# Kernel optimization log

Hardware: AMD Instinct MI355X
Metric: run time of the kernel (lower is better)

The kernel has to match this reference:

```python
import jax, jax.numpy as jnp
import numpy as np

N_NODES = 100000
N_EDGES = 1600000
F_IN = 256
HID = 16
HEADS = 8
N_CLASSES = 16
NEG_SLOPE = 0.2  # DGL GATConv default leaky_relu slope


def setup_inputs() -> dict:
    key = jax.random.key(0)
    ks = jax.random.split(key, 12)
    feat = jax.random.normal(ks[0], (N_NODES, F_IN), dtype=jnp.float32)
    src = jax.random.randint(ks[1], (N_EDGES,), 0, N_NODES, dtype=jnp.int32)
    dst = jax.random.randint(ks[2], (N_EDGES,), 0, N_NODES, dtype=jnp.int32)
    s1 = 1.0 / np.sqrt(F_IN)
    s2 = 1.0 / np.sqrt(HID * HEADS)
    W1 = jax.random.normal(ks[3], (F_IN, HEADS * HID), dtype=jnp.float32) * s1
    al1 = jax.random.normal(ks[4], (HEADS, HID), dtype=jnp.float32) * s1
    ar1 = jax.random.normal(ks[5], (HEADS, HID), dtype=jnp.float32) * s1
    b1 = jnp.zeros((HEADS * HID,), dtype=jnp.float32)
    W2 = jax.random.normal(ks[6], (HEADS * HID, N_CLASSES), dtype=jnp.float32) * s2
    al2 = jax.random.normal(ks[7], (1, N_CLASSES), dtype=jnp.float32) * s2
    ar2 = jax.random.normal(ks[8], (1, N_CLASSES), dtype=jnp.float32) * s2
    b2 = jnp.zeros((N_CLASSES,), dtype=jnp.float32)
    return {"feat": feat, "src": src, "dst": dst,
            "W1": W1, "al1": al1, "ar1": ar1, "b1": b1,
            "W2": W2, "al2": al2, "ar2": ar2, "b2": b2}


def gat_conv(x, src, dst, W, attn_l, attn_r, bias, n_heads, out_dim):
    # x: [N, F_in]; W: [F_in, H*D]; attn_l/attn_r: [H, D]; bias: [H*D]
    n = x.shape[0]
    h = (x @ W).reshape(n, n_heads, out_dim)              # [N,H,D]
    el = jnp.einsum('nhd,hd->nh', h, attn_l)              # [N,H]
    er = jnp.einsum('nhd,hd->nh', h, attn_r)              # [N,H]
    e = jax.nn.leaky_relu(el[src] + er[dst], NEG_SLOPE)   # [E,H]
    # segment softmax over incoming edges of each destination node
    e_max = jax.ops.segment_max(e, dst, num_segments=n)   # [N,H] (-inf for isolated)
    ex = jnp.exp(e - e_max[dst])                          # [E,H]
    denom = jax.ops.segment_sum(ex, dst, num_segments=n)  # [N,H]
    a = ex / denom[dst]                                   # [E,H]
    msg = a[:, :, None] * h[src]                          # [E,H,D]
    out = jax.ops.segment_sum(msg, dst, num_segments=n)   # [N,H,D]
    return out + bias.reshape(1, n_heads, out_dim)


def reference(feat, src, dst, W1, al1, ar1, b1, W2, al2, ar2, b2):
    h = gat_conv(feat, src, dst, W1, al1, ar1, b1, HEADS, HID)   # [N,H,HID]
    h = jax.nn.elu(h.reshape(h.shape[0], -1))                     # [N,H*HID]
    h = gat_conv(h, src, dst, W2, al2, ar2, b2, 1, N_CLASSES)     # [N,1,C]
    h = h.reshape(h.shape[0], -1)
    return jax.nn.log_softmax(h, axis=1)
```

## Files before the change

### kernel.cpp

```cpp
#include <hip/hip_runtime.h>

#define N_NODES 100000
#define N_EDGES 1600000
#define F_IN 256
#define HD1 128
#define HEADS 8
#define HID 16
#define NC 16
#define NEG_SLOPE 0.2f
#define LOG2E 1.44269504f

#define BKT_NODES 512
#define NBKT ((N_NODES + BKT_NODES - 1) / BKT_NODES)
#define P1_EPB 8192
#define P1_BLOCKS ((N_EDGES + P1_EPB - 1) / P1_EPB)

__device__ __forceinline__ float leaky(float x){ return x > 0.f ? x : NEG_SLOPE * x; }
__device__ __forceinline__ unsigned short f2bf(float f){
    unsigned u = __float_as_uint(f);
    u += 0x7fff + ((u >> 16) & 1);
    return (unsigned short)(u >> 16);
}
__device__ __forceinline__ float bf2f(unsigned short s){
    return __uint_as_float((unsigned)s << 16);
}
__device__ __forceinline__ unsigned char f2fp8(float v){
    return (unsigned char)(__builtin_amdgcn_cvt_pk_fp8_f32(v, v, 0, false) & 0xff);
}
__device__ __forceinline__ unsigned cvtpk_bf16(float lo, float hi){
    unsigned r;
    asm("v_cvt_pk_bf16_f32 %0, %1, %2" : "=v"(r) : "v"(lo), "v"(hi));
    return r;
}

typedef __bf16 bf16x8 __attribute__((ext_vector_type(8)));
typedef short short8 __attribute__((ext_vector_type(8)));
typedef float f32x4 __attribute__((ext_vector_type(4)));
typedef float f32x2 __attribute__((ext_vector_type(2)));


__global__ void __launch_bounds__(256) k_p1hist(const int* __restrict__ dst, int* __restrict__ bucketTotal){
    __shared__ int h[NBKT];
    int t = threadIdx.x;
    for (int i = t; i < NBKT; i += 256) h[i] = 0;
    __syncthreads();
    int base = blockIdx.x * P1_EPB;
    int m = min(P1_EPB, N_EDGES - base);
    for (int i = t; i < m; i += 256) atomicAdd(&h[(unsigned)dst[base + i] >> 9], 1);
    __syncthreads();
    for (int i = t; i < NBKT; i += 256) if (h[i]) atomicAdd(&bucketTotal[i], h[i]);
}

__global__ void __launch_bounds__(256) k_p1scan(const int* __restrict__ bucketTotal,
                                                int* __restrict__ bucketBase, int* __restrict__ bucketCursor,
                                                int* __restrict__ off){
    __shared__ int sc[256];
    int t = threadIdx.x;
    int v = (t < NBKT) ? bucketTotal[t] : 0;
    sc[t] = v; __syncthreads();
    for (int o = 1; o < 256; o <<= 1){
        int a = (t >= o) ? sc[t - o] : 0;
        __syncthreads();
        sc[t] += a;
        __syncthreads();
    }
    if (t < NBKT){
        int b = sc[t] - v;
        bucketBase[t] = b;
        bucketCursor[t] = b;
    }
    if (t == 0){ bucketBase[NBKT] = N_EDGES; off[N_NODES] = N_EDGES; }
}

__global__ void __launch_bounds__(256) k_p1bin(const int* __restrict__ src, const int* __restrict__ dst,
                                               int* __restrict__ bucketCursor,
                                               unsigned long long* __restrict__ pairs){
    __shared__ unsigned long long pl[P1_EPB];
    __shared__ int h[NBKT];
    __shared__ int dl[NBKT];
    __shared__ int sc[256];
    int t = threadIdx.x;
    for (int i = t; i < NBKT; i += 256) h[i] = 0;
    __syncthreads();
    int base = blockIdx.x * P1_EPB;
    int m = min(P1_EPB, N_EDGES - base);
    for (int i = t; i < m; i += 256) atomicAdd(&h[(unsigned)dst[base + i] >> 9], 1);
    __syncthreads();
    int v = (t < NBKT) ? h[t] : 0;
    sc[t] = v; __syncthreads();
    for (int o = 1; o < 256; o <<= 1){
        int a = (t >= o) ? sc[t - o] : 0;
        __syncthreads();
        sc[t] += a;
        __syncthreads();
    }
    if (t < NBKT){
        int ex = sc[t] - v;
        int gb = v ? atomicAdd(&bucketCursor[t], v) : 0;
        dl[t] = gb - ex;
        h[t] = ex;
    }
    __syncthreads();
    for (int i = t; i < m; i += 256){
        int d = dst[base + i], s = src[base + i];
        int b = (unsigned)d >> 9;
        int p = atomicAdd(&h[b], 1);
        pl[p] = ((unsigned long long)(unsigned)d << 32) | (unsigned)s;
    }
    __syncthreads();
    for (int i = t; i < m; i += 256){
        unsigned long long pr = pl[i];
        int b = (unsigned)(pr >> 32) >> 9;
        pairs[i + dl[b]] = pr;
    }
}

__global__ void __launch_bounds__(256) k_p2place(const unsigned long long* __restrict__ pairs,
                                                 const int* __restrict__ bucketBase,
                                                 int* __restrict__ off, int* __restrict__ csr_src){
    __shared__ int degc[BKT_NODES];
    __shared__ int sc2[BKT_NODES];
    int t = threadIdx.x;
    int b = blockIdx.x;
    int node0 = b * BKT_NODES;
    int nmax = min(BKT_NODES, N_NODES - node0);
    int p0 = bucketBase[b], p1 = bucketBase[b + 1];
    int m = p1 - p0;
    for (int i = t; i < BKT_NODES; i += 256) degc[i] = 0;
    __syncthreads();
    for (int i = t; i < m; i += 256){
        int d = (int)(pairs[p0 + i] >> 32) - node0;
        atomicAdd(&degc[d], 1);
    }
    __syncthreads();
    for (int i = t; i < BKT_NODES; i += 256) sc2[i] = degc[i];
    __syncthreads();
    for (int o = 1; o < BKT_NODES; o <<= 1){
        int i0 = t, i1 = t + 256;
        int a0 = (i0 >= o) ? sc2[i0 - o] : 0;
        int a1 = (i1 >= o) ? sc2[i1 - o] : 0;
        __syncthreads();
        sc2[i0] += a0; sc2[i1] += a1;
        __syncthreads();
    }
    for (int i = t; i < BKT_NODES; i += 256){
        int cur = p0 + sc2[i] - degc[i];
        if (i < nmax) off[node0 + i] = cur;
        degc[i] = cur;
    }
    __syncthreads();
    for (int i = t; i < m; i += 256){
        unsigned long long pr = pairs[p0 + i];
        int d = (int)(pr >> 32) - node0;
        int pos = atomicAdd(&degc[d], 1);
        csr_src[pos] = (int)(unsigned)pr;
    }
}


__global__ void __launch_bounds__(256) k_splitW(const float* __restrict__ W1,
                                                short* __restrict__ WTH){
    int i = blockIdx.x * 256 + threadIdx.x;
    if (i >= F_IN * HD1) return;
    int k = i >> 7, n = i & 127;
    int idx = n * 256 + (k ^ ((n & 7) << 3));
    WTH[idx] = (short)f2bf(W1[i]);
}


__device__ __forceinline__ short8 pack8(float4 f0, float4 f1){
    uint4 p;
    p.x = cvtpk_bf16(f0.x, f0.y);
    p.y = cvtpk_bf16(f0.z, f0.w);
    p.z = cvtpk_bf16(f1.x, f1.y);
    p.w = cvtpk_bf16(f1.z, f1.w);
    return __builtin_bit_cast(short8, p);
}

__global__ void __launch_bounds__(256, 2) k_gemm1m(const float* __restrict__ feat,
                                                   const short* __restrict__ WTH,
                                                   unsigned char* __restrict__ h1f8){
    __shared__ short sWH[64 * 256];
    int t = threadIdx.x;
    int ch = blockIdx.y;
    {
        const short8* gh = (const short8*)(WTH + (size_t)ch * 16384);
        short8* sh = (short8*)sWH;
        for (int i = t; i < 2048; i += 256) sh[i] = gh[i];
    }

    int wid = t >> 6, lane = t & 63;
    int m16 = lane & 15, kg = lane >> 4;
    int rowb = blockIdx.x * 128 + wid * 32;

    int r0 = rowb + m16;       if (r0 > N_NODES - 1) r0 = N_NODES - 1;
    int r1 = rowb + 16 + m16;  if (r1 > N_NODES - 1) r1 = N_NODES - 1;
    const float* fp0 = feat + (size_t)r0 * F_IN;
    const float* fp1 = feat + (size_t)r1 * F_IN;

    float4 s0[16], s1[16];
    #pragma unroll
    for (int ks = 0; ks < 8; ks++){
        const float4* p = (const float4*)(fp0 + ks * 32 + kg * 8);
        s0[2 * ks] = p[0]; s0[2 * ks + 1] = p[1];
    }
    #pragma unroll
    for (int ks = 0; ks < 8; ks++){
        const float4* p = (const float4*)(fp1 + ks * 32 + kg * 8);
        s1[2 * ks] = p[0]; s1[2 * ks + 1] = p[1];
    }

    __syncthreads();

    f32x4 acc[2][4];
    #pragma unroll
    for (int a = 0; a < 2; a++)
        #pragma unroll
        for (int b = 0; b < 4; b++)
            acc[a][b] = (f32x4){0.f, 0.f, 0.f, 0.f};

    #pragma unroll
    for (int ks = 0; ks < 8; ks++){
        int kbase = ks * 32 + kg * 8;
        bf16x8 AH0 = __builtin_bit_cast(bf16x8, pack8(s0[2 * ks], s0[2 * ks + 1]));
        bf16x8 AH1 = __builtin_bit_cast(bf16x8, pack8(s1[2 * ks], s1[2 * ks + 1]));
        #pragma unroll
        for (int c = 0; c < 4; c++){
            int n = (c << 4) + m16;
            int kk = kbase ^ ((n & 7) << 3);
            bf16x8 bh = __builtin_bit_cast(bf16x8, *(const short8*)(sWH + n * 256 + kk));
            acc[0][c] = __builtin_amdgcn_mfma_f32_16x16x32_bf16(AH0, bh, acc[0][c], 0, 0, 0);
            acc[1][c] = __builtin_amdgcn_mfma_f32_16x16x32_bf16(AH1, bh, acc[1][c], 0, 0, 0);
        }
    }

    #pragma unroll
    for (int rf = 0; rf < 2; rf++){
        #pragma unroll
        for (int c = 0; c < 4; c++){
            #pragma unroll
            for (int r = 0; r < 4; r++){
                int row = rowb + rf * 16 + kg * 4 + r;
                if (row < N_NODES){
                    int col = ch * 64 + c * 16 + m16;
                    h1f8[(size_t)row * HD1 + col] = f2fp8(acc[rf][c][r]);
                }
            }
        }
    }
}


__global__ void __launch_bounds__(256) k_attn1(const unsigned char* __restrict__ h1f8,
                                               const float* __restrict__ al1, const float* __restrict__ ar1,
                                               unsigned short* __restrict__ el1b, float* __restrict__ er1){
    int i = blockIdx.x * 256 + threadIdx.x;
    if (i >= N_NODES * HEADS) return;
    int n = i >> 3, h = i & 7;
    const unsigned* hp = (const unsigned*)(h1f8 + (size_t)n * HD1 + h * HID);
    float pe = 0.f, pr = 0.f;
    #pragma unroll
    for (int j = 0; j < 4; j++){
        unsigned u = hp[j];
        float x0 = __builtin_amdgcn_cvt_f32_fp8(u, 0);
        float x1 = __builtin_amdgcn_cvt_f32_fp8(u, 1);
        float x2 = __builtin_amdgcn_cvt_f32_fp8(u, 2);
        float x3 = __builtin_amdgcn_cvt_f32_fp8(u, 3);
        const float4 a = ((const float4*)(al1 + h * HID))[j];
        const float4 r = ((const float4*)(ar1 + h * HID))[j];
        pe += x0 * a.x + x1 * a.y + x2 * a.z + x3 * a.w;
        pr += x0 * r.x + x1 * r.y + x2 * r.z + x3 * r.w;
    }
    el1b[i] = f2bf(pe * LOG2E);
    er1[i] = pr * LOG2E;
}


__global__ void __launch_bounds__(256) k_agg1(const int* __restrict__ off, const int* __restrict__ csr_src,
                                              const unsigned short* __restrict__ el1b,
                                              const float* __restrict__ er1,
                                              const unsigned char* __restrict__ h1f8,
                                              const float* __restrict__ b1,
                                              unsigned short* __restrict__ x2b){
    int wid = threadIdx.x >> 6, lane = threadIdx.x & 63;
    int n = blockIdx.x * 4 + wid;
    if (n >= N_NODES) return;
    int jb = off[n], je = off[n + 1];
    int sub = lane >> 4;
    int q = lane & 15;
    int hh = q >> 1;
    float ern = er1[n * HEADS + hh];
    float a0=0.f,a1=0.f,a2=0.f,a3=0.f,a4=0.f,a5=0.f,a6=0.f,a7=0.f,wsum=0.f;

    #pragma unroll 2
    for (int j = jb; j < je; j += 4){
        int jj = j + sub;
        int jc = (jj < je) ? jj : je - 1;
        int s = csr_src[jc];
        float el = bf2f(el1b[s * HEADS + hh]);
        float wv = (jj < je) ? __builtin_amdgcn_exp2f(leaky(el + ern)) : 0.f;
        wsum += wv;
        uint2 u = *(const uint2*)(h1f8 + (((size_t)s) << 7) + (q << 3));
        f32x2 p0 = __builtin_amdgcn_cvt_pk_f32_fp8(u.x, 0);
        f32x2 p1 = __builtin_amdgcn_cvt_pk_f32_fp8(u.x, 1);
        f32x2 p2 = __builtin_amdgcn_cvt_pk_f32_fp8(u.y, 0);
        f32x2 p3 = __builtin_amdgcn_cvt_pk_f32_fp8(u.y, 1);
        a0 += wv * p0.x; a1 += wv * p0.y;
        a2 += wv * p1.x; a3 += wv * p1.y;
        a4 += wv * p2.x; a5 += wv * p2.y;
        a6 += wv * p3.x; a7 += wv * p3.y;
    }

    a0 += __shfl_xor(a0, 16); a0 += __shfl_xor(a0, 32);
    a1 += __shfl_xor(a1, 16); a1 += __shfl_xor(a1, 32);
    a2 += __shfl_xor(a2, 16); a2 += __shfl_xor(a2, 32);
    a3 += __shfl_xor(a3, 16); a3 += __shfl_xor(a3, 32);
    a4 += __shfl_xor(a4, 16); a4 += __shfl_xor(a4, 32);
    a5 += __shfl_xor(a5, 16); a5 += __shfl_xor(a5, 32);
    a6 += __shfl_xor(a6, 16); a6 += __shfl_xor(a6, 32);
    a7 += __shfl_xor(a7, 16); a7 += __shfl_xor(a7, 32);
    wsum += __shfl_xor(wsum, 16); wsum += __shfl_xor(wsum, 32);

    if (sub == 0){
        float inv = (je > jb) ? 1.f / wsum : 0.f;
        float o0 = a0*inv, o1 = a1*inv, o2 = a2*inv, o3 = a3*inv;
        float o4 = a4*inv, o5 = a5*inv, o6 = a6*inv, o7 = a7*inv;
        float4 bv0 = *(const float4*)(b1 + (q << 3));
        float4 bv1 = *(const float4*)(b1 + (q << 3) + 4);
        o0 += bv0.x; o1 += bv0.y; o2 += bv0.z; o3 += bv0.w;
        o4 += bv1.x; o5 += bv1.y; o6 += bv1.z; o7 += bv1.w;
        o0 = o0 > 0.f ? o0 : __expf(o0) - 1.f;
        o1 = o1 > 0.f ? o1 : __expf(o1) - 1.f;
        o2 = o2 > 0.f ? o2 : __expf(o2) - 1.f;
        o3 = o3 > 0.f ? o3 : __expf(o3) - 1.f;
        o4 = o4 > 0.f ? o4 : __expf(o4) - 1.f;
        o5 = o5 > 0.f ? o5 : __expf(o5) - 1.f;
        o6 = o6 > 0.f ? o6 : __expf(o6) - 1.f;
        o7 = o7 > 0.f ? o7 : __expf(o7) - 1.f;
        uint4 ov;
        ov.x = cvtpk_bf16(o0, o1);
        ov.y = cvtpk_bf16(o2, o3);
        ov.z = cvtpk_bf16(o4, o5);
        ov.w = cvtpk_bf16(o6, o7);
        *(uint4*)(x2b + (size_t)n * HD1 + (q << 3)) = ov;
    }
}


__global__ void __launch_bounds__(256) k_gemm2(const unsigned short* __restrict__ x2b, const float* __restrict__ W2,
                                               const float* __restrict__ al2, const float* __restrict__ ar2,
                                               unsigned short* __restrict__ h2b, float* __restrict__ el2, float* __restrict__ er2){
    __shared__ float sW[HD1 * NC];
    __shared__ float sX[16 * HD1];
    int t = threadIdx.x;
    for (int i = t; i < (HD1 * NC) / 4; i += 256)
        ((float4*)sW)[i] = ((const float4*)W2)[i];
    int r = t >> 4, c = t & 15;
    float a2 = al2[c], r2 = ar2[c];
    for (int g = blockIdx.x; g * 16 < N_NODES; g += gridDim.x){
        int rowb = g * 16;
        __syncthreads();
        {
            ushort4 v = ((const ushort4*)(x2b + (size_t)rowb * HD1))[t * 2];
            ushort4 v2 = ((const ushort4*)(x2b + (size_t)rowb * HD1))[t * 2 + 1];
            float4 f0 = { bf2f(v.x), bf2f(v.y), bf2f(v.z), bf2f(v.w) };
            float4 f1 = { bf2f(v2.x), bf2f(v2.y), bf2f(v2.z), bf2f(v2.w) };
            ((float4*)sX)[t * 2] = f0;
            ((float4*)sX)[t * 2 + 1] = f1;
        }
        __syncthreads();
        float acc = 0.f;
        #pragma unroll 8
        for (int k = 0; k < HD1; k++)
            acc += sX[r * HD1 + k] * sW[k * NC + c];
        int row = rowb + r;
        h2b[row * NC + c] = f2bf(acc);
        float pe = acc * a2, pr = acc * r2;
        #pragma unroll
        for (int d = 1; d < 16; d <<= 1){ pe += __shfl_xor(pe, d); pr += __shfl_xor(pr, d); }
        if (c == 0){ el2[row] = pe * LOG2E; er2[row] = pr * LOG2E; }
    }
}


__global__ void __launch_bounds__(256) k_agg2(const int* __restrict__ off, const int* __restrict__ csr_src,
                                              const float* __restrict__ el2, const float* __restrict__ er2,
                                              const unsigned short* __restrict__ h2b, const float* __restrict__ b2,
                                              float* __restrict__ out){
    int t = threadIdx.x;
    int sub = t >> 4;
    int c = t & 15;
    int n = blockIdx.x * 16 + sub;
    if (n >= N_NODES) return;
    int jb = off[n], je = off[n + 1];
    float er = er2[n];
    float accA = 0.f, accB = 0.f, wsA = 0.f, wsB = 0.f;
    int j = jb;
    for (; j + 1 < je; j += 2){
        int s0 = csr_src[j];
        int s1 = csr_src[j + 1];
        float w0 = __builtin_amdgcn_exp2f(leaky(el2[s0] + er));
        float w1 = __builtin_amdgcn_exp2f(leaky(el2[s1] + er));
        float v0 = bf2f(h2b[(size_t)s0 * NC + c]);
        float v1 = bf2f(h2b[(size_t)s1 * NC + c]);
        wsA += w0; accA += w0 * v0;
        wsB += w1; accB += w1 * v1;
    }
    if (j < je){
        int s0 = csr_src[j];
        float w0 = __builtin_amdgcn_exp2f(leaky(el2[s0] + er));
        wsA += w0; accA += w0 * bf2f(h2b[(size_t)s0 * NC + c]);
    }
    float acc = accA + accB, wsum = wsA + wsB;
    float o = (je > jb) ? acc / wsum : 0.f;
    o += b2[c];
    float m = o;
    #pragma unroll
    for (int d = 1; d < 16; d <<= 1) m = fmaxf(m, __shfl_xor(m, d));
    float ex = __expf(o - m);
    #pragma unroll
    for (int d = 1; d < 16; d <<= 1) ex += __shfl_xor(ex, d);
    out[(size_t)n * NC + c] = o - m - __logf(ex);
}


extern "C" void kernel_launch(void* const* d_in, const int* in_sizes, int n_in,
                              void* d_out, int out_size, void* d_ws, size_t ws_size,
                              hipStream_t stream){
    const float* feat = (const float*)d_in[0];
    const int*   src  = (const int*)d_in[1];
    const int*   dst  = (const int*)d_in[2];
    const float* W1   = (const float*)d_in[3];
    const float* al1  = (const float*)d_in[4];
    const float* ar1  = (const float*)d_in[5];
    const float* b1   = (const float*)d_in[6];
    const float* W2   = (const float*)d_in[7];
    const float* al2  = (const float*)d_in[8];
    const float* ar2  = (const float*)d_in[9];
    const float* b2   = (const float*)d_in[10];
    float* out = (float*)d_out;

    char* w = (char*)d_ws;
    auto alloc = [&](size_t bytes) -> char* {
        char* p = w;
        w += (bytes + 255) & ~(size_t)255;
        return p;
    };
    int*   off      = (int*)alloc((size_t)(N_NODES + 1) * 4);
    int*   csr_src  = (int*)alloc((size_t)N_EDGES * 4);
    unsigned long long* pairs = (unsigned long long*)alloc((size_t)N_EDGES * 8);
    int*   bucketTotal  = (int*)alloc((size_t)(NBKT + 1) * 4);
    int*   bucketBase   = (int*)alloc((size_t)(NBKT + 1) * 4);
    int*   bucketCursor = (int*)alloc((size_t)(NBKT + 1) * 4);
    unsigned char*  h1f8 = (unsigned char*)alloc((size_t)N_NODES * HD1);
    unsigned short* el1b = (unsigned short*)alloc((size_t)N_NODES * HEADS * 2);
    float* er1v    = (float*)alloc((size_t)N_NODES * HEADS * 4);
    unsigned short* x2b = (unsigned short*)alloc((size_t)N_NODES * HD1 * 2);
    unsigned short* h2b = (unsigned short*)alloc((size_t)N_NODES * NC * 2);
    float* el2v    = (float*)alloc((size_t)N_NODES * 4);
    float* er2v    = (float*)alloc((size_t)N_NODES * 4);
    short* WTH     = (short*)alloc((size_t)F_IN * HD1 * 2);

    hipMemsetAsync(bucketTotal, 0, (size_t)(NBKT + 1) * 4, stream);
    k_p1hist<<<P1_BLOCKS, 256, 0, stream>>>(dst, bucketTotal);
    k_p1scan<<<1, 256, 0, stream>>>(bucketTotal, bucketBase, bucketCursor, off);
    k_p1bin<<<P1_BLOCKS, 256, 0, stream>>>(src, dst, bucketCursor, pairs);
    k_p2place<<<NBKT, 256, 0, stream>>>(pairs, bucketBase, off, csr_src);

    k_splitW<<<(F_IN * HD1 + 255) / 256, 256, 0, stream>>>(W1, WTH);
    dim3 g1((N_NODES + 127) / 128, 2);
    k_gemm1m<<<g1, 256, 0, stream>>>(feat, WTH, h1f8);
    k_attn1<<<(N_NODES * HEADS + 255) / 256, 256, 0, stream>>>(h1f8, al1, ar1, el1b, er1v);

    k_agg1<<<(N_NODES + 3) / 4, 256, 0, stream>>>(off, csr_src, el1b, er1v, h1f8, b1, x2b);

    k_gemm2<<<1024, 256, 0, stream>>>(x2b, W2, al2, ar2, h2b, el2v, er2v);
    k_agg2<<<(N_NODES + 15) / 16, 256, 0, stream>>>(off, csr_src, el2v, er2v, h2b, b2, out);
}
```

Measured before the change: 234.1 us.

## Compute all 128 GEMM1 columns per block with LDS-staged, double-buffered features

The first-layer GEMM now has each block compute all 128 output columns instead of splitting them across two column-chunk blocks, so each feature row is read from global memory once rather than twice. Feature tiles are streamed into a swizzled, double-buffered LDS array using direct global-to-LDS loads, which replaces the large per-thread register prefetch. The costs are a larger LDS footprint (the full bf16 weight plus two feature buffers, about 96KB), which limits occupancy, a __syncthreads per k-step, and twice as many accumulators per wave.

```diff
diff --git a/kernel.cpp b/kernel.cpp
--- a/kernel.cpp
+++ b/kernel.cpp
@@ -32,6 +32,11 @@
     asm("v_cvt_pk_bf16_f32 %0, %1, %2" : "=v"(r) : "v"(lo), "v"(hi));
     return r;
 }
+__device__ __forceinline__ void gload_lds16(const float* g, float* l){
+    __builtin_amdgcn_global_load_lds(
+        (const __attribute__((address_space(1))) unsigned int*)g,
+        (__attribute__((address_space(3))) unsigned int*)l, 16, 0, 0);
+}
 
 typedef __bf16 bf16x8 __attribute__((ext_vector_type(8)));
 typedef short short8 __attribute__((ext_vector_type(8)));
@@ -177,72 +182,82 @@
     return __builtin_bit_cast(short8, p);
 }
 
-__global__ void __launch_bounds__(256, 2) k_gemm1m(const float* __restrict__ feat,
-                                                   const short* __restrict__ WTH,
-                                                   unsigned char* __restrict__ h1f8){
-    __shared__ short sWH[64 * 256];
-    int t = threadIdx.x;
-    int ch = blockIdx.y;
+__global__ void __launch_bounds__(256) k_gemm1m(const float* __restrict__ feat,
+                                                const short* __restrict__ WTH,
+                                                unsigned char* __restrict__ h1f8){
+    __shared__ short sWH[F_IN * HD1];
+    __shared__ float sF[2][4096];
+    int t = threadIdx.x;
     {
-        const short8* gh = (const short8*)(WTH + (size_t)ch * 16384);
+        const short8* gh = (const short8*)WTH;
         short8* sh = (short8*)sWH;
-        for (int i = t; i < 2048; i += 256) sh[i] = gh[i];
+        for (int i = t; i < 4096; i += 256) sh[i] = gh[i];
     }
 
     int wid = t >> 6, lane = t & 63;
     int m16 = lane & 15, kg = lane >> 4;
-    int rowb = blockIdx.x * 128 + wid * 32;
-
-    int r0 = rowb + m16;       if (r0 > N_NODES - 1) r0 = N_NODES - 1;
-    int r1 = rowb + 16 + m16;  if (r1 > N_NODES - 1) r1 = N_NODES - 1;
-    const float* fp0 = feat + (size_t)r0 * F_IN;
-    const float* fp1 = feat + (size_t)r1 * F_IN;
-
-    float4 s0[16], s1[16];
-    #pragma unroll
-    for (int ks = 0; ks < 8; ks++){
-        const float4* p = (const float4*)(fp0 + ks * 32 + kg * 8);
-        s0[2 * ks] = p[0]; s0[2 * ks + 1] = p[1];
-    }
-    #pragma unroll
-    for (int ks = 0; ks < 8; ks++){
-        const float4* p = (const float4*)(fp1 + ks * 32 + kg * 8);
-        s1[2 * ks] = p[0]; s1[2 * ks + 1] = p[1];
-    }
-
-    __syncthreads();
-
-    f32x4 acc[2][4];
+    int rowb = blockIdx.x * 128;
+
+    int srow = lane >> 3;
+    int scg  = (lane & 7) ^ srow;
+
+    auto stage = [&](int ks, int b){
+        #pragma unroll
+        for (int i = 0; i < 4; i++){
+            int reg = wid * 4 + i;
+            int grow = rowb + reg * 8 + srow;
+            if (grow > N_NODES - 1) grow = N_NODES - 1;
+            const float* gp = feat + (size_t)grow * F_IN + ks * 32 + scg * 4;
+            gload_lds16(gp, &sF[b][reg * 256]);
+        }
+    };
+
+    stage(0, 0);
+    __syncthreads();
+
+    f32x4 acc[2][8];
     #pragma unroll
     for (int a = 0; a < 2; a++)
         #pragma unroll
-        for (int b = 0; b < 4; b++)
-            acc[a][b] = (f32x4){0.f, 0.f, 0.f, 0.f};
+        for (int c = 0; c < 8; c++)
+            acc[a][c] = (f32x4){0.f, 0.f, 0.f, 0.f};
+
+    int rA0 = wid * 32 + m16, rA1 = rA0 + 16;
+    int sw = m16 & 7;
 
     #pragma unroll
     for (int ks = 0; ks < 8; ks++){
+        int b = ks & 1;
+        if (ks < 7) stage(ks + 1, b ^ 1);
+        const float* fb = sF[b];
+        float4 a00 = *(const float4*)(fb + rA0 * 32 + (((2 * kg) ^ sw) << 2));
+        float4 a01 = *(const float4*)(fb + rA0 * 32 + (((2 * kg + 1) ^ sw) << 2));
+        float4 a10 = *(const float4*)(fb + rA1 * 32 + (((2 * kg) ^ sw) << 2));
+        float4 a11 = *(const float4*)(fb + rA1 * 32 + (((2 * kg + 1) ^ sw) << 2));
+        bf16x8 AH0 = __builtin_bit_cast(bf16x8, pack8(a00, a01));
+        bf16x8 AH1 = __builtin_bit_cast(bf16x8, pack8(a10, a11));
         int kbase = ks * 32 + kg * 8;
-        bf16x8 AH0 = __builtin_bit_cast(bf16x8, pack8(s0[2 * ks], s0[2 * ks + 1]));
-        bf16x8 AH1 = __builtin_bit_cast(bf16x8, pack8(s1[2 * ks], s1[2 * ks + 1]));
         #pragma unroll
-        for (int c = 0; c < 4; c++){
+        for (int c = 0; c < 8; c++){
             int n = (c << 4) + m16;
             int kk = kbase ^ ((n & 7) << 3);
             bf16x8 bh = __builtin_bit_cast(bf16x8, *(const short8*)(sWH + n * 256 + kk));
             acc[0][c] = __builtin_amdgcn_mfma_f32_16x16x32_bf16(AH0, bh, acc[0][c], 0, 0, 0);
             acc[1][c] = __builtin_amdgcn_mfma_f32_16x16x32_bf16(AH1, bh, acc[1][c], 0, 0, 0);
         }
-    }
-
+        __syncthreads();
+    }
+
+    int wrow = rowb + wid * 32;
     #pragma unroll
     for (int rf = 0; rf < 2; rf++){
         #pragma unroll
-        for (int c = 0; c < 4; c++){
+        for (int c = 0; c < 8; c++){
             #pragma unroll
             for (int r = 0; r < 4; r++){
-                int row = rowb + rf * 16 + kg * 4 + r;
+                int row = wrow + rf * 16 + kg * 4 + r;
                 if (row < N_NODES){
-                    int col = ch * 64 + c * 16 + m16;
+                    int col = c * 16 + m16;
                     h1f8[(size_t)row * HD1 + col] = f2fp8(acc[rf][c][r]);
                 }
             }
@@ -468,8 +483,7 @@
     k_p2place<<<NBKT, 256, 0, stream>>>(pairs, bucketBase, off, csr_src);
 
     k_splitW<<<(F_IN * HD1 + 255) / 256, 256, 0, stream>>>(W1, WTH);
-    dim3 g1((N_NODES + 127) / 128, 2);
-    k_gemm1m<<<g1, 256, 0, stream>>>(feat, WTH, h1f8);
+    k_gemm1m<<<(N_NODES + 127) / 128, 256, 0, stream>>>(feat, WTH, h1f8);
     k_attn1<<<(N_NODES * HEADS + 255) / 256, 256, 0, stream>>>(h1f8, al1, ar1, el1b, er1v);
 
     k_agg1<<<(N_NODES + 3) / 4, 256, 0, stream>>>(off, csr_src, el1b, er1v, h1f8, b1, x2b);
```

Result: slower. 246.4 us (+5.3%).
